# Performance work log

Measured on AMD Instinct MI355X. Metric: run time of the kernel, lower is better.

Reference implementation:

```python
import jax, jax.numpy as jnp
import numpy as np

# PointPillars KITTI grid
NX, NY, NZ = 432, 496, 1
C = 64            # num_bev_features
B = 8             # batch size
P_PER = 4096      # pillars per sample (<=4096 -> deterministic path, no gumbel gating)
GRID = NZ * NX * NY


def setup_inputs() -> dict:
    key = jax.random.key(0)
    pillar_features = jax.random.normal(key, (B * P_PER, C), dtype=jnp.float32)
    # Unique flat indices per sample: stride 53 is coprime with NX*NY=214272,
    # and P_PER < NX*NY, so all indices within a sample are distinct (scatter-set safe).
    flat = (np.arange(P_PER, dtype=np.int64) * 53) % (NX * NY)
    ys = flat // NX
    xs = flat % NX
    coords = np.stack([
        np.repeat(np.arange(B, dtype=np.int64), P_PER),  # batch index
        np.zeros(B * P_PER, dtype=np.int64),             # z (always 0, nz==1)
        np.tile(ys, B),                                  # y
        np.tile(xs, B),                                  # x
    ], axis=1)
    return {
        "pillar_features": pillar_features,
        "voxel_coords": jnp.asarray(coords, dtype=jnp.int32),
    }


def reference(pillar_features, voxel_coords):
    c = voxel_coords.astype(jnp.int32)
    # per-sample flat index into the nz*nx*ny canvas: z + y*nx + x
    idx = c[:, 1] + c[:, 2] * NX + c[:, 3]
    # fold batch into a single global scatter (one kernel instead of a per-batch loop)
    gidx = c[:, 0] * GRID + idx                       # [P]
    canvas = jnp.zeros((B * GRID, C), dtype=pillar_features.dtype)
    canvas = canvas.at[gidx].set(pillar_features)     # sparse-to-dense scatter
    # [B*GRID, C] -> [B, GRID, C] -> [B, C, GRID] -> [B, C*nz, ny, nx]
    out = canvas.reshape(B, GRID, C).transpose(0, 2, 1).reshape(B, C * NZ, NY, NX)
    return out
```

## Files before the change

kernel.cpp:

```cpp
#include <hip/hip_runtime.h>


#define PPS_NX   432
#define PPS_NY   496
#define PPS_GRID (PPS_NX * PPS_NY)
#define PPS_C    64
#define PPS_B    8
#define PPS_U    (PPS_GRID / 4)

typedef float f32x4 __attribute__((ext_vector_type(4)));

__global__ void pps_init_map(int4* __restrict__ map4, int n4) {
    int i = blockIdx.x * blockDim.x + threadIdx.x;
    if (i < n4) map4[i] = make_int4(-1, -1, -1, -1);
}

__global__ void pps_scatter_idx(const int4* __restrict__ coords,
                                int* __restrict__ map, int P) {
    int p = blockIdx.x * blockDim.x + threadIdx.x;
    if (p >= P) return;
    int4 c = coords[p];
    int pos = c.y + c.z * PPS_NX + c.w;
    map[c.x * PPS_GRID + pos] = p;
}

__global__ __launch_bounds__(256) void pps_write(const float* __restrict__ pf,
                                                 const int* __restrict__ map,
                                                 f32x4* __restrict__ out4) {
    int f = blockIdx.x * 256 + threadIdx.x;
    int plane = (unsigned)f / PPS_U;
    int u = f - plane * PPS_U;
    int b = plane >> 6;
    int ch = plane & 63;

    const int4 m = ((const int4*)(map + (size_t)b * PPS_GRID))[u];

    f32x4 v = {0.f, 0.f, 0.f, 0.f};
    if ((m.x & m.y & m.z & m.w) >= 0) {
        if (m.x >= 0) v.x = pf[(size_t)m.x * PPS_C + ch];
        if (m.y >= 0) v.y = pf[(size_t)m.y * PPS_C + ch];
        if (m.z >= 0) v.z = pf[(size_t)m.z * PPS_C + ch];
        if (m.w >= 0) v.w = pf[(size_t)m.w * PPS_C + ch];
    }
    out4[f] = v;
}

__global__ void pps_zero_out(float4* __restrict__ out, long long n4) {
    long long i = (long long)blockIdx.x * blockDim.x + threadIdx.x;
    const long long stride = (long long)gridDim.x * blockDim.x;
    const float4 z = make_float4(0.f, 0.f, 0.f, 0.f);
    for (; i < n4; i += stride) out[i] = z;
}
__global__ void pps_scatter_feat(const float* __restrict__ pf,
                                 const int4* __restrict__ coords,
                                 float* __restrict__ out, int P) {
    int t = blockIdx.x * blockDim.x + threadIdx.x;
    int p = t >> 6;
    if (p >= P) return;
    int ch = t & 63;
    int4 c = coords[p];
    long long pos = (long long)c.x * (long long)(PPS_C * PPS_GRID)
                  + (long long)ch * PPS_GRID
                  + (long long)(c.y + c.z * PPS_NX + c.w);
    out[pos] = pf[t];
}

extern "C" void kernel_launch(void* const* d_in, const int* in_sizes, int n_in,
                              void* d_out, int out_size, void* d_ws, size_t ws_size,
                              hipStream_t stream) {
    const float* pf     = (const float*)d_in[0];
    const int4*  coords = (const int4*)d_in[1];
    float*       out    = (float*)d_out;
    int P = in_sizes[0] / PPS_C;

    const size_t map_bytes = (size_t)PPS_B * PPS_GRID * sizeof(int);
    if (ws_size >= map_bytes) {
        int* map = (int*)d_ws;
        int n4 = PPS_B * PPS_U;
        pps_init_map<<<(n4 + 255) / 256, 256, 0, stream>>>((int4*)map, n4);
        pps_scatter_idx<<<(P + 255) / 256, 256, 0, stream>>>(coords, map, P);
        int total4 = out_size / 4;
        pps_write<<<total4 / 256, 256, 0, stream>>>(pf, map, (f32x4*)out);
    } else {
        long long n4 = (long long)out_size / 4;
        pps_zero_out<<<2048, 256, 0, stream>>>((float4*)out, n4);
        int threads = P * PPS_C;
        pps_scatter_feat<<<(threads + 255) / 256, 256, 0, stream>>>(pf, coords, out, P);
    }
}
```

Baseline: 435.9 us.

## Compose output per spatial slice with pillar rows staged in shared memory

Replaces the per-plane write kernel with one where each block owns a 256-float4 spatial slice of one batch and loops over all 64 channels. The block reads the map once, compacts the occupied pillars into shared-memory slots, loads each pillar's 64-float row once with coalesced vector loads, and then emits the channel planes from shared memory. This removes the 64-fold rereading of the map and the strided per-channel gathers from pillar features. The cost is fewer, longer blocks, atomics on shared memory, and a fallback for slices holding more than 64 pillars.

```diff
diff --git a/kernel.cpp b/kernel.cpp
--- a/kernel.cpp
+++ b/kernel.cpp
@@ -7,6 +7,10 @@
 #define PPS_C    64
 #define PPS_B    8
 #define PPS_U    (PPS_GRID / 4)
+#define SLICE_F4 256
+#define N_SLICE  ((PPS_U + SLICE_F4 - 1) / SLICE_F4)
+#define MAX_SLOTS 64
+#define ROW_PITCH 65
 
 typedef float f32x4 __attribute__((ext_vector_type(4)));
 
@@ -24,25 +28,67 @@
     map[c.x * PPS_GRID + pos] = p;
 }
 
-__global__ __launch_bounds__(256) void pps_write(const float* __restrict__ pf,
-                                                 const int* __restrict__ map,
-                                                 f32x4* __restrict__ out4) {
-    int f = blockIdx.x * 256 + threadIdx.x;
-    int plane = (unsigned)f / PPS_U;
-    int u = f - plane * PPS_U;
-    int b = plane >> 6;
-    int ch = plane & 63;
+__global__ __launch_bounds__(256) void pps_compose(const float* __restrict__ pf,
+                                                   const int* __restrict__ map,
+                                                   f32x4* __restrict__ out4) {
+    __shared__ float rows[MAX_SLOTS * ROW_PITCH];
+    __shared__ int   slotPillar[MAX_SLOTS];
+    __shared__ int   nSlots;
 
-    const int4 m = ((const int4*)(map + (size_t)b * PPS_GRID))[u];
+    const int slice = blockIdx.x;
+    const int b     = blockIdx.y;
+    const int t     = threadIdx.x;
+    const int u     = slice * SLICE_F4 + t;
+    const bool inb  = (u < PPS_U);
 
-    f32x4 v = {0.f, 0.f, 0.f, 0.f};
-    if ((m.x & m.y & m.z & m.w) >= 0) {
-        if (m.x >= 0) v.x = pf[(size_t)m.x * PPS_C + ch];
-        if (m.y >= 0) v.y = pf[(size_t)m.y * PPS_C + ch];
-        if (m.z >= 0) v.z = pf[(size_t)m.z * PPS_C + ch];
-        if (m.w >= 0) v.w = pf[(size_t)m.w * PPS_C + ch];
+    if (t == 0) nSlots = 0;
+
+    int4 m = make_int4(-1, -1, -1, -1);
+    if (inb) m = ((const int4*)(map + (size_t)b * PPS_GRID))[u];
+    __syncthreads();
+
+    int s0 = -1, s1 = -1, s2 = -1, s3 = -1;
+    if (m.x >= 0) { int s = atomicAdd(&nSlots, 1); if (s < MAX_SLOTS) { slotPillar[s] = m.x; s0 = s; } else s0 = -2; }
+    if (m.y >= 0) { int s = atomicAdd(&nSlots, 1); if (s < MAX_SLOTS) { slotPillar[s] = m.y; s1 = s; } else s1 = -2; }
+    if (m.z >= 0) { int s = atomicAdd(&nSlots, 1); if (s < MAX_SLOTS) { slotPillar[s] = m.z; s2 = s; } else s2 = -2; }
+    if (m.w >= 0) { int s = atomicAdd(&nSlots, 1); if (s < MAX_SLOTS) { slotPillar[s] = m.w; s3 = s; } else s3 = -2; }
+    __syncthreads();
+
+    int S = nSlots; if (S > MAX_SLOTS) S = MAX_SLOTS;
+    for (int idx = t; idx < S * 16; idx += 256) {
+        int slot = idx >> 4, j = idx & 15;
+        f32x4 r = ((const f32x4*)pf)[(size_t)slotPillar[slot] * 16 + j];
+        float* dst = rows + slot * ROW_PITCH + j * 4;
+        dst[0] = r.x; dst[1] = r.y; dst[2] = r.z; dst[3] = r.w;
     }
-    out4[f] = v;
+    __syncthreads();
+
+    if (!inb) return;
+
+    size_t base = (size_t)b * (64 * (size_t)PPS_U) + u;
+    const f32x4 z4 = {0.f, 0.f, 0.f, 0.f};
+
+    if (((s0 & s1) & (s2 & s3)) == -1) {
+        #pragma unroll
+        for (int ch = 0; ch < PPS_C; ++ch) {
+            out4[base] = z4;
+            base += PPS_U;
+        }
+    } else {
+        for (int ch = 0; ch < PPS_C; ++ch) {
+            f32x4 v = z4;
+            if (s0 >= 0) v.x = rows[s0 * ROW_PITCH + ch];
+            else if (s0 == -2) v.x = pf[(size_t)m.x * PPS_C + ch];
+            if (s1 >= 0) v.y = rows[s1 * ROW_PITCH + ch];
+            else if (s1 == -2) v.y = pf[(size_t)m.y * PPS_C + ch];
+            if (s2 >= 0) v.z = rows[s2 * ROW_PITCH + ch];
+            else if (s2 == -2) v.z = pf[(size_t)m.z * PPS_C + ch];
+            if (s3 >= 0) v.w = rows[s3 * ROW_PITCH + ch];
+            else if (s3 == -2) v.w = pf[(size_t)m.w * PPS_C + ch];
+            out4[base] = v;
+            base += PPS_U;
+        }
+    }
 }
 
 __global__ void pps_zero_out(float4* __restrict__ out, long long n4) {
@@ -76,11 +122,11 @@
     const size_t map_bytes = (size_t)PPS_B * PPS_GRID * sizeof(int);
     if (ws_size >= map_bytes) {
         int* map = (int*)d_ws;
-        int n4 = PPS_B * PPS_U;
+        int n4 = PPS_B * (PPS_GRID / 4);
         pps_init_map<<<(n4 + 255) / 256, 256, 0, stream>>>((int4*)map, n4);
         pps_scatter_idx<<<(P + 255) / 256, 256, 0, stream>>>(coords, map, P);
-        int total4 = out_size / 4;
-        pps_write<<<total4 / 256, 256, 0, stream>>>(pf, map, (f32x4*)out);
+        dim3 grid(N_SLICE, PPS_B);
+        pps_compose<<<grid, 256, 0, stream>>>(pf, map, (f32x4*)out);
     } else {
         long long n4 = (long long)out_size / 4;
         pps_zero_out<<<2048, 256, 0, stream>>>((float4*)out, n4);
```

Measured after the change: 616.2 us. +41.4%, slower.
